# Performance work log

Hardware: AMD Instinct MI355X
Metric: run time of the kernel (lower is better)

Reference implementation:

```python
import jax, jax.numpy as jnp
import numpy as np

N, F, D = 32, 1024, 512
H = 2 * D  # dim * ratio
EPS = 1e-5


def batchnorm1d(x, gamma, beta):
    # x: (N, F, L); BatchNorm1d over channel dim F, stats over (N, L) (training mode, biased var)
    mean = jnp.mean(x, axis=(0, 2), keepdims=True)
    var = jnp.var(x, axis=(0, 2), keepdims=True)
    xn = (x - mean) * jax.lax.rsqrt(var + EPS)
    return xn * gamma[None, :, None] + beta[None, :, None]


def setup_inputs() -> dict:
    key = jax.random.key(0)
    ks = jax.random.split(key, 5)
    x = jax.random.normal(ks[0], (N, F, D), dtype=jnp.float32)
    W0 = jax.random.normal(ks[1], (H, D), dtype=jnp.float32) * 0.02  # Linear(D->H) weight (out,in)
    b0 = jnp.zeros((H,), jnp.float32)
    W1 = jax.random.normal(ks[2], (D, H), dtype=jnp.float32) * 0.02  # Linear(H->D)
    b1 = jnp.zeros((D,), jnp.float32)
    Wc = jax.random.normal(ks[3], (F, F), dtype=jnp.float32) * 0.02  # Conv1d k=1 weight (out_ch,in_ch)
    bc = jnp.zeros((F,), jnp.float32)
    ones = jnp.ones((F,), jnp.float32)
    zeros = jnp.zeros((F,), jnp.float32)
    return {
        "x": x,
        "W0": W0, "b0": b0, "g0": ones, "be0": zeros,
        "W1": W1, "b1": b1, "g1": ones, "be1": zeros,
        "gf": ones, "bf": zeros,
        "Wc": Wc, "bc": bc,
        "go": ones, "bo": zeros,
    }


def reference(x, W0, b0, g0, be0, W1, b1, g1, be1, gf, bf, Wc, bc, go, bo):
    # proj_mlp0: Linear(D->H) + BN1d(F)
    v = jnp.einsum('nfd,hd->nfh', x, W0) + b0  # (N, F, H)
    v = batchnorm1d(v, g0, be0)
    # correlation: bmm(v, v^T) -> softsign -> bmm(w, v)
    w = jnp.einsum('nfh,ngh->nfg', v, v)  # (N, F, F)
    w = w / (1.0 + jnp.abs(w))  # softsign
    v = jnp.einsum('nfg,ngh->nfh', w, v)  # (N, F, H)
    # proj_mlp1: Linear(H->D) + BN1d(F)
    v = jnp.einsum('nfh,dh->nfd', v, W1) + b1  # (N, F, D)
    v = batchnorm1d(v, g1, be1)
    # feed_norm(v + x)
    xr = batchnorm1d(v + x, gf, bf)
    # proj_conv: Conv1d(F->F, kernel=1) over channel dim
    v = jnp.einsum('oi,nid->nod', Wc, xr) + bc[None, :, None]
    return batchnorm1d(v + xr, go, bo)
```

## Files before the change

### kernel.cpp

```cpp
#include <hip/hip_runtime.h>
#include <stdint.h>

#define NB 32
#define FC 1024
#define DD 512
#define HH 1024
#define BN_EPS 1e-5f

typedef unsigned short u16;
typedef unsigned int u32;
typedef __attribute__((ext_vector_type(8))) short bf16x8;
typedef __attribute__((ext_vector_type(4))) float f32x4;
typedef __attribute__((ext_vector_type(8))) unsigned short ushort8v;

#define AS1 __attribute__((address_space(1)))
#define AS3 __attribute__((address_space(3)))

__device__ __forceinline__ float b2f(u16 u) {
    union { u32 i; float f; } v;
    v.i = ((u32)u) << 16;
    return v.f;
}
__device__ __forceinline__ u16 f2b(float f) {
    union { float f; u32 i; } v;
    v.f = f;
    const u32 b = v.i;
    return (u16)((b + 0x7FFFu + ((b >> 16) & 1u)) >> 16);
}

__device__ __forceinline__ void gld16(const u16* g, u16* l) {
    __builtin_amdgcn_global_load_lds((const AS1 u32*)g, (AS3 u32*)l, 16, 0, 0);
}

__device__ __forceinline__ void swizzle_tiles(int& mt, int& nt, int& zt) {
    const int gx = gridDim.x, gy = gridDim.y, gz = gridDim.z;
    const int mzTot = gy * gz;
    if ((mzTot & 7) != 0) { nt = blockIdx.x; mt = blockIdx.y; zt = blockIdx.z; return; }
    long lin = ((long)blockIdx.z * gy + blockIdx.y) * gx + blockIdx.x;
    const int slab = mzTot >> 3;
    const int xcd = (int)(lin & 7);
    const long idx = lin >> 3;
    nt = (int)(idx % gx);
    const int mz = (int)(idx / gx) + xcd * slab;
    mt = mz % gy;
    zt = mz / gy;
}

__global__ __launch_bounds__(256) void init_detect(
    float* __restrict__ sp, const u32* __restrict__ x, int* __restrict__ flag)
{
    sp[blockIdx.x * 256 + threadIdx.x] = 0.0f;
    if (blockIdx.x != 0) return;
    __shared__ int cnt[256];
    int c = 0;
    for (int i = threadIdx.x; i < 4096; i += 256) {
        const u32 lo = x[i] & 0xFFFFu;
        const u32 e = (lo >> 7) & 0xFFu;
        if (e >= 0x68u && e <= 0x85u) c++;
    }
    cnt[threadIdx.x] = c;
    __syncthreads();
    for (int s = 128; s > 0; s >>= 1) {
        if (threadIdx.x < (unsigned)s) cnt[threadIdx.x] += cnt[threadIdx.x + s];
        __syncthreads();
    }
    if (threadIdx.x == 0) flag[0] = (cnt[0] > 2048) ? 1 : 0;
}

__global__ __launch_bounds__(256) void fold_bn(
    const float* __restrict__ sp, const u16* __restrict__ gamma,
    const u16* __restrict__ beta, float* __restrict__ ssf, float invCnt)
{
    const int f = blockIdx.x * 256 + threadIdx.x;
    if (f < FC) {
        const float mean = sp[f] * invCnt;
        const float var  = sp[FC + f] * invCnt - mean * mean;
        const float rstd = rsqrtf(var + BN_EPS);
        const float sc   = b2f(gamma[f]) * rstd;
        ssf[f]      = sc;
        ssf[FC + f] = b2f(beta[f]) - mean * sc;
    }
}

__global__ __launch_bounds__(256) void fold2_bn(
    const float* __restrict__ sp1, const float* __restrict__ spx,
    const u16* __restrict__ g1, const u16* __restrict__ be1,
    const u16* __restrict__ gf, const u16* __restrict__ bf_,
    float* __restrict__ ssd, float cnt)
{
    const int f = blockIdx.x * 256 + threadIdx.x;
    if (f >= FC) return;
    const float inv  = 1.0f / cnt;
    const float S1v = sp1[f], S2v = sp1[FC + f], Sxv = sp1[2 * FC + f];
    const float mean1 = S1v * inv;
    const float var1  = S2v * inv - mean1 * mean1;
    const float sc1   = b2f(g1[f]) * rsqrtf(var1 + BN_EPS);
    const float sh1   = b2f(be1[f]) - mean1 * sc1;
    ssd[f]      = sc1;
    ssd[FC + f] = sh1;
    const float S1x = spx[f], S2x = spx[FC + f];
    const float sums = sc1 * S1v + cnt * sh1 + S1x;
    const float sss  = sc1 * sc1 * S2v + 2.f * sc1 * sh1 * S1v
                     + cnt * sh1 * sh1 + 2.f * sc1 * Sxv
                     + 2.f * sh1 * S1x + S2x;
    const float means = sums * inv;
    const float vars  = sss * inv - means * means;
    const float scf   = b2f(gf[f]) * rsqrtf(vars + BN_EPS);
    const float shf   = b2f(bf_[f]) - means * scf;
    ssd[2 * FC + f] = scf;
    ssd[3 * FC + f] = shf;
}

__global__ __launch_bounds__(256) void convert_x_stats(
    const void* __restrict__ src, u16* __restrict__ dst, long n4,
    const int* __restrict__ flag, float* __restrict__ spx)
{
    const bool isbf = (*flag != 0);
    long i4 = (long)blockIdx.x * blockDim.x + threadIdx.x;
    const long stride = (long)gridDim.x * blockDim.x;
    for (; i4 < n4; i4 += stride) {
        const long i = i4 << 2;
        ushort4 o;
        if (isbf) {
            o = *(const ushort4*)((const u16*)src + i);
        } else {
            const float4 v = *(const float4*)((const float*)src + i);
            o.x = f2b(v.x); o.y = f2b(v.y); o.z = f2b(v.z); o.w = f2b(v.w);
        }
        *(ushort4*)(dst + i) = o;
        const float a = b2f(o.x), b = b2f(o.y), c = b2f(o.z), d = b2f(o.w);
        float s1 = a + b + c + d;
        float s2 = a * a + b * b + c * c + d * d;
        #pragma unroll
        for (int m = 1; m < 64; m <<= 1) {
            s1 += __shfl_xor(s1, m);
            s2 += __shfl_xor(s2, m);
        }
        if ((threadIdx.x & 63) == 0) {
            const int ch = (int)((i >> 9) & (FC - 1));
            atomicAdd(&spx[ch], s1);
            atomicAdd(&spx[FC + ch], s2);
        }
    }
}

struct ConvArgs { const void* src[14]; long off[14]; long n4[14]; };
__global__ __launch_bounds__(256) void convert_params(
    ConvArgs a, u16* __restrict__ dst, const int* __restrict__ flag)
{
    const bool isbf = (*flag != 0);
    const long stride = (long)gridDim.x * blockDim.x;
    for (int s = 0; s < 14; ++s) {
        const long n4 = a.n4[s];
        u16* d = dst + a.off[s];
        const void* sp = a.src[s];
        for (long i4 = (long)blockIdx.x * blockDim.x + threadIdx.x; i4 < n4;
             i4 += stride) {
            const long i = i4 << 2;
            if (isbf) {
                *(ushort4*)(d + i) = *(const ushort4*)((const u16*)sp + i);
            } else {
                const float4 v = *(const float4*)((const float*)sp + i);
                ushort4 o;
                o.x = f2b(v.x); o.y = f2b(v.y); o.z = f2b(v.z); o.w = f2b(v.w);
                *(ushort4*)(d + i) = o;
            }
        }
    }
}

template<bool BIAS, bool SOFTSIGN, bool STATS, bool RESID, bool XSTAT>
__global__ __launch_bounds__(512, 4) void gemm128x256_nt(
    const u16* __restrict__ A, const u16* __restrict__ B,
    const u16* __restrict__ bias, const u16* __restrict__ resid,
    u16* __restrict__ C, float* __restrict__ sp,
    int M, int N, int K, int lda, int ldb, int ldc,
    long sA, long sB, long sC)
{
    extern __shared__ char smem[];

    int mt, nt, zt;
    swizzle_tiles(mt, nt, zt);
    const u16* Ab = A + (long)zt * sA + (long)(mt * 128) * lda;
    const u16* Bb = B + (long)zt * sB + (long)(nt * 256) * ldb;
    C += (long)zt * sC;
    const u16* RP = (RESID || XSTAT) ? (resid + (long)zt * sC) : nullptr;

    const int tid  = threadIdx.x;
    const int lane = tid & 63;
    const int wv   = tid >> 6;
    const int wrr  = (wv >> 2) * 64;
    const int wc   = (wv & 3) * 64;
    const int lm   = lane & 15;
    const int q    = lane >> 4;

    int aOff[4], bOff[4];
    #pragma unroll
    for (int i = 0; i < 4; ++i) {
        const int r = wrr + i * 16 + lm;
        aOff[i] = r * 64 + ((q ^ ((r >> 1) & 3)) << 4);
    }
    #pragma unroll
    for (int j = 0; j < 4; ++j) {
        const int r = wc + j * 16 + lm;
        bOff[j] = r * 64 + ((q ^ ((r >> 1) & 3)) << 4);
    }

    const int rw = lane >> 2, qs = lane & 3;
    const int rA  = wv * 16 + rw;
    const int rB0 = wv * 32 + rw;
    const int rB1 = wv * 32 + 16 + rw;
    const u16* pA  = Ab + (long)rA  * lda + ((qs ^ ((rA  >> 1) & 3)) << 3);
    const u16* pB0 = Bb + (long)rB0 * ldb + ((qs ^ ((rB0 >> 1) & 3)) << 3);
    const u16* pB1 = Bb + (long)rB1 * ldb + ((qs ^ ((rB1 >> 1) & 3)) << 3);
    const int ldsA  = wv * 1024;
    const int ldsB0 = wv * 2048;
    const int ldsB1 = wv * 2048 + 1024;

#define STAGE(bufOff, kofs) { \
    gld16(pA  + (kofs), (u16*)(smem + (bufOff) + ldsA)); \
    gld16(pB0 + (kofs), (u16*)(smem + (bufOff) + 8192 + ldsB0)); \
    gld16(pB1 + (kofs), (u16*)(smem + (bufOff) + 8192 + ldsB1)); }

    f32x4 acc[4][4] = {};

    const int NT = K >> 5;

    STAGE(0, 0);
    __syncthreads();

    for (int t = 0; t < NT; ++t) {
        const int bo = (t & 1) * 24576;
        const int bn = ((t + 1) & 1) * 24576;
        if (t + 1 < NT) STAGE(bn, (t + 1) * 32);

        bf16x8 a[4], b[4];
        const char* baseA = smem + bo;
        const char* baseB = smem + bo + 8192;
        #pragma unroll
        for (int i = 0; i < 4; ++i) a[i] = *(const bf16x8*)(baseA + aOff[i]);
        #pragma unroll
        for (int j = 0; j < 4; ++j) b[j] = *(const bf16x8*)(baseB + bOff[j]);

        #pragma unroll
        for (int i = 0; i < 4; ++i)
            #pragma unroll
            for (int j = 0; j < 4; ++j)
                acc[i][j] = __builtin_amdgcn_mfma_f32_16x16x32_bf16(
                    a[i], b[j], acc[i][j], 0, 0, 0);

        __syncthreads();
    }

#undef STAGE

    float* rep = (float*)smem + wv * (16 * 65);
    const int rr = lane >> 2;
    const int cg = lane & 3;
    const int m0 = mt * 128;
    const int n0 = nt * 256;
    #pragma unroll
    for (int i = 0; i < 4; ++i) {
        #pragma unroll
        for (int j = 0; j < 4; ++j) {
            const int col = 16 * j + lm;
            const float bj = BIAS ? b2f(bias[n0 + wc + col]) : 0.0f;
            #pragma unroll
            for (int r = 0; r < 4; ++r) {
                float v = acc[i][j][r] + bj;
                if (SOFTSIGN) v = v / (1.0f + fabsf(v));
                rep[(q * 4 + r) * 65 + col] = v;
            }
        }
        const int row = m0 + wrr + 16 * i + rr;
        const float* lr = rep + rr * 65 + cg * 16;
        float4 f0 = *(const float4*)(lr + 0);
        float4 f1 = *(const float4*)(lr + 4);
        float4 f2 = *(const float4*)(lr + 8);
        float4 f3 = *(const float4*)(lr + 12);
        ushort8v ra, rb;
        if (RESID || XSTAT) {
            const u16* rp = RP + (long)row * ldc + n0 + wc + cg * 16;
            ra = *(const ushort8v*)rp;
            rb = *(const ushort8v*)(rp + 8);
        }
        if (RESID) {
            f0.x += b2f(ra[0]); f0.y += b2f(ra[1]); f0.z += b2f(ra[2]); f0.w += b2f(ra[3]);
            f1.x += b2f(ra[4]); f1.y += b2f(ra[5]); f1.z += b2f(ra[6]); f1.w += b2f(ra[7]);
            f2.x += b2f(rb[0]); f2.y += b2f(rb[1]); f2.z += b2f(rb[2]); f2.w += b2f(rb[3]);
            f3.x += b2f(rb[4]); f3.y += b2f(rb[5]); f3.z += b2f(rb[6]); f3.w += b2f(rb[7]);
        }
        if (STATS) {
            float s1 = (f0.x + f0.y + f0.z + f0.w) + (f1.x + f1.y + f1.z + f1.w)
                     + (f2.x + f2.y + f2.z + f2.w) + (f3.x + f3.y + f3.z + f3.w);
            float s2 = f0.x*f0.x + f0.y*f0.y + f0.z*f0.z + f0.w*f0.w
                     + f1.x*f1.x + f1.y*f1.y + f1.z*f1.z + f1.w*f1.w
                     + f2.x*f2.x + f2.y*f2.y + f2.z*f2.z + f2.w*f2.w
                     + f3.x*f3.x + f3.y*f3.y + f3.z*f3.z + f3.w*f3.w;
            float sxv = 0.0f;
            if (XSTAT) {
                sxv = f0.x*b2f(ra[0]) + f0.y*b2f(ra[1]) + f0.z*b2f(ra[2]) + f0.w*b2f(ra[3])
                    + f1.x*b2f(ra[4]) + f1.y*b2f(ra[5]) + f1.z*b2f(ra[6]) + f1.w*b2f(ra[7])
                    + f2.x*b2f(rb[0]) + f2.y*b2f(rb[1]) + f2.z*b2f(rb[2]) + f2.w*b2f(rb[3])
                    + f3.x*b2f(rb[4]) + f3.y*b2f(rb[5]) + f3.z*b2f(rb[6]) + f3.w*b2f(rb[7]);
            }
            s1 += __shfl_xor(s1, 1); s1 += __shfl_xor(s1, 2);
            s2 += __shfl_xor(s2, 1); s2 += __shfl_xor(s2, 2);
            if (XSTAT) { sxv += __shfl_xor(sxv, 1); sxv += __shfl_xor(sxv, 2); }
            if (cg == 0) {
                const int ch = row & (FC - 1);
                atomicAdd(&sp[ch], s1);
                atomicAdd(&sp[FC + ch], s2);
                if (XSTAT) atomicAdd(&sp[2 * FC + ch], sxv);
            }
        }
        ushort8v o0, o1;
        o0[0] = f2b(f0.x); o0[1] = f2b(f0.y); o0[2] = f2b(f0.z); o0[3] = f2b(f0.w);
        o0[4] = f2b(f1.x); o0[5] = f2b(f1.y); o0[6] = f2b(f1.z); o0[7] = f2b(f1.w);
        o1[0] = f2b(f2.x); o1[1] = f2b(f2.y); o1[2] = f2b(f2.z); o1[3] = f2b(f2.w);
        o1[4] = f2b(f3.x); o1[5] = f2b(f3.y); o1[6] = f2b(f3.z); o1[7] = f2b(f3.w);
        u16* cp = C + (long)row * ldc + n0 + wc + cg * 16;
        *(ushort8v*)cp = o0;
        *(ushort8v*)(cp + 8) = o1;
    }
}

__global__ __launch_bounds__(256) void transpose_bn_bf16(
    const u16* __restrict__ src, u16* __restrict__ dstT,
    u16* __restrict__ dstI, const float* __restrict__ ssf,
    int R, int Cc, long sS, long sD)
{
    __shared__ u16 t[32][36];
    const int bz = blockIdx.z;
    src  += (long)bz * sS;
    dstI += (long)bz * sS;
    dstT += (long)bz * sD;
    const int c0 = blockIdx.x * 32;
    const int r0 = blockIdx.y * 32;
    const int lx = threadIdx.x & 7;
    const int ly = threadIdx.x >> 3;

    const int r = r0 + ly;
    const float sc = ssf[r];
    const float sh = ssf[FC + r];
    const ushort4 v = *(const ushort4*)(src + (long)r * Cc + c0 + lx * 4);
    ushort4 nv;
    nv.x = f2b(fmaf(b2f(v.x), sc, sh));
    nv.y = f2b(fmaf(b2f(v.y), sc, sh));
    nv.z = f2b(fmaf(b2f(v.z), sc, sh));
    nv.w = f2b(fmaf(b2f(v.w), sc, sh));
    *(ushort4*)(dstI + (long)r * Cc + c0 + lx * 4) = nv;
    *(ushort4*)&t[ly][lx * 4] = nv;

    __syncthreads();

    const int oc = c0 + ly;
    ushort4 o;
    o.x = t[lx * 4 + 0][ly];
    o.y = t[lx * 4 + 1][ly];
    o.z = t[lx * 4 + 2][ly];
    o.w = t[lx * 4 + 3][ly];
    *(ushort4*)(dstT + (long)oc * R + r0 + lx * 4) = o;
}

__global__ __launch_bounds__(256) void transpose_bn2_bf16(
    const u16* __restrict__ v3, const u16* __restrict__ x,
    u16* __restrict__ dstT, u16* __restrict__ dstI,
    const float* __restrict__ ssd, int R, int Cc, long sS, long sD)
{
    __shared__ u16 t[32][36];
    const int bz = blockIdx.z;
    v3   += (long)bz * sS;
    x    += (long)bz * sS;
    dstI += (long)bz * sS;
    dstT += (long)bz * sD;
    const int c0 = blockIdx.x * 32;
    const int r0 = blockIdx.y * 32;
    const int lx = threadIdx.x & 7;
    const int ly = threadIdx.x >> 3;

    const int r = r0 + ly;
    const float sc1 = ssd[r];
    const float sh1 = ssd[FC + r];
    const float scf = ssd[2 * FC + r];
    const float shf = ssd[3 * FC + r];
    const long base = (long)r * Cc + c0 + lx * 4;
    const ushort4 v  = *(const ushort4*)(v3 + base);
    const ushort4 xv = *(const ushort4*)(x + base);
    ushort4 nv;
    float s;
    s = fmaf(b2f(v.x), sc1, sh1) + b2f(xv.x); nv.x = f2b(fmaf(s, scf, shf));
    s = fmaf(b2f(v.y), sc1, sh1) + b2f(xv.y); nv.y = f2b(fmaf(s, scf, shf));
    s = fmaf(b2f(v.z), sc1, sh1) + b2f(xv.z); nv.z = f2b(fmaf(s, scf, shf));
    s = fmaf(b2f(v.w), sc1, sh1) + b2f(xv.w); nv.w = f2b(fmaf(s, scf, shf));
    *(ushort4*)(dstI + base) = nv;
    *(ushort4*)&t[ly][lx * 4] = nv;

    __syncthreads();

    const int oc = c0 + ly;
    ushort4 o;
    o.x = t[lx * 4 + 0][ly];
    o.y = t[lx * 4 + 1][ly];
    o.z = t[lx * 4 + 2][ly];
    o.w = t[lx * 4 + 3][ly];
    *(ushort4*)(dstT + (long)oc * R + r0 + lx * 4) = o;
}

__global__ __launch_bounds__(256) void bn_apply(
    const u16* __restrict__ src, const float* __restrict__ ss,
    void* __restrict__ dst, const int* __restrict__ outflag,
    long total4, int lcShift)
{
    const bool outf32 = (outflag != nullptr) && (*outflag == 0);
    long i4 = (long)blockIdx.x * blockDim.x + threadIdx.x;
    const long stride = (long)gridDim.x * blockDim.x;
    for (; i4 < total4; i4 += stride) {
        const long i = i4 << 2;
        const int c = (int)((i >> lcShift) & (FC - 1));
        const float sc = ss[c];
        const float sh = ss[FC + c];
        const ushort4 v = *(const ushort4*)(src + i);
        const float o0 = fmaf(b2f(v.x), sc, sh);
        const float o1 = fmaf(b2f(v.y), sc, sh);
        const float o2 = fmaf(b2f(v.z), sc, sh);
        const float o3 = fmaf(b2f(v.w), sc, sh);
        if (outf32) {
            float4 o; o.x = o0; o.y = o1; o.z = o2; o.w = o3;
            *(float4*)((float*)dst + i) = o;
        } else {
            ushort4 o;
            o.x = f2b(o0); o.y = f2b(o1); o.z = f2b(o2); o.w = f2b(o3);
            *(ushort4*)((u16*)dst + i) = o;
        }
    }
}

extern "C" void kernel_launch(void* const* d_in, const int* in_sizes, int n_in,
                              void* d_out, int out_size, void* d_ws, size_t ws_size,
                              hipStream_t stream)
{
    const size_t MiB = (size_t)1 << 20;
    const long sFH = (long)FC * HH;
    const long sFF = (long)FC * FC;
    const long sFD = (long)FC * DD;
    const long PE  = (long)NB * FC * DD;

    const size_t GLDS = 49152;
    static bool s_attr = false;
    if (!s_attr) {
        s_attr = true;
        hipFuncSetAttribute(reinterpret_cast<const void*>(&gemm128x256_nt<true, false, true, false, false>),
                            hipFuncAttributeMaxDynamicSharedMemorySize, (int)GLDS);
        hipFuncSetAttribute(reinterpret_cast<const void*>(&gemm128x256_nt<false, true, false, false, false>),
                            hipFuncAttributeMaxDynamicSharedMemorySize, (int)GLDS);
        hipFuncSetAttribute(reinterpret_cast<const void*>(&gemm128x256_nt<false, false, false, false, false>),
                            hipFuncAttributeMaxDynamicSharedMemorySize, (int)GLDS);
        hipFuncSetAttribute(reinterpret_cast<const void*>(&gemm128x256_nt<true, false, true, false, true>),
                            hipFuncAttributeMaxDynamicSharedMemorySize, (int)GLDS);
        hipFuncSetAttribute(reinterpret_cast<const void*>(&gemm128x256_nt<true, false, true, true, false>),
                            hipFuncAttributeMaxDynamicSharedMemorySize, (int)GLDS);
    }

    long off[16];
    long cur = 0;
    for (int i = 1; i < 15; ++i) { off[i] = cur; cur += ((long)in_sizes[i] + 7) & ~7L; }
    const size_t paramBytes = (size_t)cur * 2;

    int cb = 32;
    while (cb > 1 &&
           64 * MiB + (size_t)cb * 6 * MiB + paramBytes + 131072 > ws_size)
        cb >>= 1;

    u16* V   = (u16*)d_ws;
    u16* VT  = (u16*)((char*)d_ws + 64 * MiB);
    u16* WW  = VT + (long)cb * sFH;
    u16* V2  = WW + (long)cb * sFF;
    u16* WC  = V2 + (long)cb * sFH;
    char* tail = (char*)(WC + cur);
    tail = (char*)(((uintptr_t)tail + 255) & ~(uintptr_t)255);
    float* SP0  = (float*)tail;
    float* SP1  = SP0 + 2 * FC;
    float* SPX  = SP1 + 3 * FC;
    float* SP3  = SPX + 2 * FC;
    float* SSF  = SP3 + 2 * FC;
    float* SSD  = SSF + 2 * FC;
    int*   FLAG = (int*)(SSD + 4 * FC);
    u16* VX  = (u16*)d_out;
    u16* XB  = (u16*)d_out + PE;
    u16* V4  = V;
    u16* XRT = V + PE;

    const dim3 blk(256);
    const dim3 blk512(512);
    const dim3 egrid(4096);

    init_detect<<<dim3(36), blk, 0, stream>>>(SP0, (const u32*)d_in[0], FLAG);
    ConvArgs ca;
    for (int i = 1; i < 15; ++i) {
        ca.src[i - 1] = d_in[i];
        ca.off[i - 1] = off[i];
        ca.n4[i - 1]  = (long)in_sizes[i] / 4;
    }
    convert_params<<<dim3(256), blk, 0, stream>>>(ca, WC, FLAG);
    convert_x_stats<<<dim3(1024), blk, 0, stream>>>(d_in[0], XB, PE / 4, FLAG, SPX);

    const u16* W0c = WC + off[1];
    const u16* b0c = WC + off[2];
    const u16* g0c = WC + off[3];
    const u16* be0c = WC + off[4];
    const u16* W1c = WC + off[5];
    const u16* b1c = WC + off[6];
    const u16* g1c = WC + off[7];
    const u16* be1c = WC + off[8];
    const u16* gfc = WC + off[9];
    const u16* bfc = WC + off[10];
    const u16* Wcc = WC + off[11];
    const u16* bcc = WC + off[12];
    const u16* goc = WC + off[13];
    const u16* boc = WC + off[14];

    gemm128x256_nt<true, false, true, false, false><<<dim3(HH / 256, (NB * FC) / 128, 1), blk512, GLDS, stream>>>(
        XB, W0c, b0c, nullptr, V, SP0, NB * FC, HH, DD, DD, DD, HH, 0, 0, 0);
    fold_bn<<<dim3(4), blk, 0, stream>>>(SP0, g0c, be0c, SSF, 1.0f / (float)(NB * HH));

    for (int bz0 = 0; bz0 < NB; bz0 += cb) {
        const int c = (NB - bz0 < cb) ? (NB - bz0) : cb;
        transpose_bn_bf16<<<dim3(HH / 32, FC / 32, c), blk, 0, stream>>>(
            V + bz0 * sFH, VT, V + bz0 * sFH, SSF, FC, HH, sFH, sFH);
        gemm128x256_nt<false, true, false, false, false><<<dim3(FC / 256, FC / 128, c), blk512, GLDS, stream>>>(
            V + bz0 * sFH, V + bz0 * sFH, nullptr, nullptr, WW, nullptr,
            FC, FC, HH, HH, HH, FC, sFH, sFH, sFF);
        gemm128x256_nt<false, false, false, false, false><<<dim3(HH / 256, FC / 128, c), blk512, GLDS, stream>>>(
            WW, VT, nullptr, nullptr, V2, nullptr,
            FC, HH, FC, FC, FC, HH, sFF, sFH, sFH);
        gemm128x256_nt<true, false, true, false, true><<<dim3(DD / 256, (c * FC) / 128, 1), blk512, GLDS, stream>>>(
            V2, W1c, b1c, XB + bz0 * sFD, VX + bz0 * sFD, SP1,
            c * FC, DD, HH, HH, HH, DD, 0, 0, 0);
    }

    fold2_bn<<<dim3(4), blk, 0, stream>>>(SP1, SPX, g1c, be1c, gfc, bfc,
                                          SSD, (float)(NB * DD));

    transpose_bn2_bf16<<<dim3(DD / 32, FC / 32, NB), blk, 0, stream>>>(
        VX, XB, XRT, VX, SSD, FC, DD, sFD, sFD);

    gemm128x256_nt<true, false, true, true, false><<<dim3(DD / 256, FC / 128, NB), blk512, GLDS, stream>>>(
        Wcc, XRT, bcc, VX, V4, SP3, FC, DD, FC, FC, FC, DD, 0, sFD, sFD);
    fold_bn<<<dim3(4), blk, 0, stream>>>(SP3, goc, boc, SSF, 1.0f / (float)(NB * DD));

    bn_apply<<<egrid, blk, 0, stream>>>(V4, SSF, d_out, FLAG, PE / 4, 9);
}
```

Before: 591.5 us.

## Enlarge GEMM tiles to 256x256 with BK=64 and split staging

Replaces the 128x256 tile GEMM with a 256x256 tile that uses a 64-wide K step. A and B staging is split across two half-steps, with a new XOR LDS swizzle and s_setprio around the MFMA block. The aim is more MFMA work per byte loaded and fewer K-loop syncs. In exchange it uses 128KB of LDS and more accumulator registers, which lowers occupancy to about one block per CU, and halves the grid size.

Result: no change. 596.2 us (+0.8%).

```diff
diff --git a/kernel.cpp b/kernel.cpp
--- a/kernel.cpp
+++ b/kernel.cpp
@@ -170,7 +170,7 @@
 }
 
 template<bool BIAS, bool SOFTSIGN, bool STATS, bool RESID, bool XSTAT>
-__global__ __launch_bounds__(512, 4) void gemm128x256_nt(
+__global__ __launch_bounds__(512, 2) void gemm256_nt(
     const u16* __restrict__ A, const u16* __restrict__ B,
     const u16* __restrict__ bias, const u16* __restrict__ resid,
     u16* __restrict__ C, float* __restrict__ sp,
@@ -181,7 +181,7 @@
 
     int mt, nt, zt;
     swizzle_tiles(mt, nt, zt);
-    const u16* Ab = A + (long)zt * sA + (long)(mt * 128) * lda;
+    const u16* Ab = A + (long)zt * sA + (long)(mt * 256) * lda;
     const u16* Bb = B + (long)zt * sB + (long)(nt * 256) * ldb;
     C += (long)zt * sC;
     const u16* RP = (RESID || XSTAT) ? (resid + (long)zt * sC) : nullptr;
@@ -189,78 +189,94 @@
     const int tid  = threadIdx.x;
     const int lane = tid & 63;
     const int wv   = tid >> 6;
-    const int wrr  = (wv >> 2) * 64;
+    const int wr   = (wv >> 2) * 128;
     const int wc   = (wv & 3) * 64;
     const int lm   = lane & 15;
     const int q    = lane >> 4;
 
-    int aOff[4], bOff[4];
+    int aOff[8][2], bOff[4][2];
     #pragma unroll
-    for (int i = 0; i < 4; ++i) {
-        const int r = wrr + i * 16 + lm;
-        aOff[i] = r * 64 + ((q ^ ((r >> 1) & 3)) << 4);
+    for (int i = 0; i < 8; ++i) {
+        const int r = wr + i * 16 + lm;
+        #pragma unroll
+        for (int kh = 0; kh < 2; ++kh)
+            aOff[i][kh] = r * 128 + (((kh * 4 + q) ^ (r & 7)) << 4);
     }
     #pragma unroll
     for (int j = 0; j < 4; ++j) {
         const int r = wc + j * 16 + lm;
-        bOff[j] = r * 64 + ((q ^ ((r >> 1) & 3)) << 4);
-    }
-
-    const int rw = lane >> 2, qs = lane & 3;
-    const int rA  = wv * 16 + rw;
-    const int rB0 = wv * 32 + rw;
-    const int rB1 = wv * 32 + 16 + rw;
-    const u16* pA  = Ab + (long)rA  * lda + ((qs ^ ((rA  >> 1) & 3)) << 3);
-    const u16* pB0 = Bb + (long)rB0 * ldb + ((qs ^ ((rB0 >> 1) & 3)) << 3);
-    const u16* pB1 = Bb + (long)rB1 * ldb + ((qs ^ ((rB1 >> 1) & 3)) << 3);
-    const int ldsA  = wv * 1024;
-    const int ldsB0 = wv * 2048;
-    const int ldsB1 = wv * 2048 + 1024;
-
-#define STAGE(bufOff, kofs) { \
-    gld16(pA  + (kofs), (u16*)(smem + (bufOff) + ldsA)); \
-    gld16(pB0 + (kofs), (u16*)(smem + (bufOff) + 8192 + ldsB0)); \
-    gld16(pB1 + (kofs), (u16*)(smem + (bufOff) + 8192 + ldsB1)); }
-
-    f32x4 acc[4][4] = {};
-
-    const int NT = K >> 5;
-
-    STAGE(0, 0);
+        #pragma unroll
+        for (int kh = 0; kh < 2; ++kh)
+            bOff[j][kh] = r * 128 + (((kh * 4 + q) ^ (r & 7)) << 4);
+    }
+
+    const int rL  = lane >> 3;
+    const int gsw = ((lane & 7) ^ rL) << 3;
+    const u16* pAs = Ab + (long)(wv * 32 + rL) * lda + gsw;
+    const u16* pBs = Bb + (long)(wv * 32 + rL) * ldb + gsw;
+    const int ldsRow0 = wv * 32 * 128;
+
+#define STAGE_A(bufOff, kofs) { \
+    gld16(pAs + 0 * 8 * lda + (kofs), (u16*)(smem + (bufOff) + ldsRow0 + 0 * 1024)); \
+    gld16(pAs + 1 * 8 * lda + (kofs), (u16*)(smem + (bufOff) + ldsRow0 + 1 * 1024)); \
+    gld16(pAs + 2 * 8 * lda + (kofs), (u16*)(smem + (bufOff) + ldsRow0 + 2 * 1024)); \
+    gld16(pAs + 3 * 8 * lda + (kofs), (u16*)(smem + (bufOff) + ldsRow0 + 3 * 1024)); }
+#define STAGE_B(bufOff, kofs) { \
+    gld16(pBs + 0 * 8 * ldb + (kofs), (u16*)(smem + (bufOff) + 32768 + ldsRow0 + 0 * 1024)); \
+    gld16(pBs + 1 * 8 * ldb + (kofs), (u16*)(smem + (bufOff) + 32768 + ldsRow0 + 1 * 1024)); \
+    gld16(pBs + 2 * 8 * ldb + (kofs), (u16*)(smem + (bufOff) + 32768 + ldsRow0 + 2 * 1024)); \
+    gld16(pBs + 3 * 8 * ldb + (kofs), (u16*)(smem + (bufOff) + 32768 + ldsRow0 + 3 * 1024)); }
+
+    f32x4 acc[8][4] = {};
+
+    const int NT = K >> 6;
+
+    STAGE_A(0, 0); STAGE_B(0, 0);
     __syncthreads();
 
     for (int t = 0; t < NT; ++t) {
-        const int bo = (t & 1) * 24576;
-        const int bn = ((t + 1) & 1) * 24576;
-        if (t + 1 < NT) STAGE(bn, (t + 1) * 32);
-
-        bf16x8 a[4], b[4];
-        const char* baseA = smem + bo;
-        const char* baseB = smem + bo + 8192;
+        const int bo = (t & 1) * 65536;
+        const int bn = ((t + 1) & 1) * 65536;
+        const int kn = (t + 1) * 64;
+        const bool pf = (t + 1 < NT);
+
         #pragma unroll
-        for (int i = 0; i < 4; ++i) a[i] = *(const bf16x8*)(baseA + aOff[i]);
-        #pragma unroll
-        for (int j = 0; j < 4; ++j) b[j] = *(const bf16x8*)(baseB + bOff[j]);
-
-        #pragma unroll
-        for (int i = 0; i < 4; ++i)
+        for (int kh = 0; kh < 2; ++kh) {
+            if (pf) {
+                if (kh == 0) STAGE_A(bn, kn)
+                else         STAGE_B(bn, kn)
+            }
+            bf16x8 a[8], b[4];
+            const char* baseA = smem + bo;
+            const char* baseB = smem + bo + 32768;
             #pragma unroll
-            for (int j = 0; j < 4; ++j)
-                acc[i][j] = __builtin_amdgcn_mfma_f32_16x16x32_bf16(
-                    a[i], b[j], acc[i][j], 0, 0, 0);
+            for (int i = 0; i < 8; ++i) a[i] = *(const bf16x8*)(baseA + aOff[i][kh]);
+            #pragma unroll
+            for (int j = 0; j < 4; ++j) b[j] = *(const bf16x8*)(baseB + bOff[j][kh]);
+
+            __builtin_amdgcn_s_setprio(1);
+            #pragma unroll
+            for (int i = 0; i < 8; ++i)
+                #pragma unroll
+                for (int j = 0; j < 4; ++j)
+                    acc[i][j] = __builtin_amdgcn_mfma_f32_16x16x32_bf16(
+                        a[i], b[j], acc[i][j], 0, 0, 0);
+            __builtin_amdgcn_s_setprio(0);
+        }
 
         __syncthreads();
     }
 
-#undef STAGE
+#undef STAGE_A
+#undef STAGE_B
 
     float* rep = (float*)smem + wv * (16 * 65);
     const int rr = lane >> 2;
     const int cg = lane & 3;
-    const int m0 = mt * 128;
+    const int m0 = mt * 256;
     const int n0 = nt * 256;
     #pragma unroll
-    for (int i = 0; i < 4; ++i) {
+    for (int i = 0; i < 8; ++i) {
         #pragma unroll
         for (int j = 0; j < 4; ++j) {
             const int col = 16 * j + lm;
@@ -272,7 +288,7 @@
                 rep[(q * 4 + r) * 65 + col] = v;
             }
         }
-        const int row = m0 + wrr + 16 * i + rr;
+        const int row = m0 + wr + 16 * i + rr;
         const float* lr = rep + rr * 65 + cg * 16;
         float4 f0 = *(const float4*)(lr + 0);
         float4 f1 = *(const float4*)(lr + 4);
@@ -446,19 +462,19 @@
     const long sFD = (long)FC * DD;
     const long PE  = (long)NB * FC * DD;
 
-    const size_t GLDS = 49152;
+    const size_t GLDS = 131072;
     static bool s_attr = false;
     if (!s_attr) {
         s_attr = true;
-        hipFuncSetAttribute(reinterpret_cast<const void*>(&gemm128x256_nt<true, false, true, false, false>),
+        hipFuncSetAttribute(reinterpret_cast<const void*>(&gemm256_nt<true, false, true, false, false>),
                             hipFuncAttributeMaxDynamicSharedMemorySize, (int)GLDS);
-        hipFuncSetAttribute(reinterpret_cast<const void*>(&gemm128x256_nt<false, true, false, false, false>),
+        hipFuncSetAttribute(reinterpret_cast<const void*>(&gemm256_nt<false, true, false, false, false>),
                             hipFuncAttributeMaxDynamicSharedMemorySize, (int)GLDS);
-        hipFuncSetAttribute(reinterpret_cast<const void*>(&gemm128x256_nt<false, false, false, false, false>),
+        hipFuncSetAttribute(reinterpret_cast<const void*>(&gemm256_nt<false, false, false, false, false>),
                             hipFuncAttributeMaxDynamicSharedMemorySize, (int)GLDS);
-        hipFuncSetAttribute(reinterpret_cast<const void*>(&gemm128x256_nt<true, false, true, false, true>),
+        hipFuncSetAttribute(reinterpret_cast<const void*>(&gemm256_nt<true, false, true, false, true>),
                             hipFuncAttributeMaxDynamicSharedMemorySize, (int)GLDS);
-        hipFuncSetAttribute(reinterpret_cast<const void*>(&gemm128x256_nt<true, false, true, true, false>),
+        hipFuncSetAttribute(reinterpret_cast<const void*>(&gemm256_nt<true, false, true, true, false>),
                             hipFuncAttributeMaxDynamicSharedMemorySize, (int)GLDS);
     }
 
@@ -520,7 +536,7 @@
     const u16* goc = WC + off[13];
     const u16* boc = WC + off[14];
 
-    gemm128x256_nt<true, false, true, false, false><<<dim3(HH / 256, (NB * FC) / 128, 1), blk512, GLDS, stream>>>(
+    gemm256_nt<true, false, true, false, false><<<dim3(HH / 256, (NB * FC) / 256, 1), blk512, GLDS, stream>>>(
         XB, W0c, b0c, nullptr, V, SP0, NB * FC, HH, DD, DD, DD, HH, 0, 0, 0);
     fold_bn<<<dim3(4), blk, 0, stream>>>(SP0, g0c, be0c, SSF, 1.0f / (float)(NB * HH));
 
@@ -528,13 +544,13 @@
         const int c = (NB - bz0 < cb) ? (NB - bz0) : cb;
         transpose_bn_bf16<<<dim3(HH / 32, FC / 32, c), blk, 0, stream>>>(
             V + bz0 * sFH, VT, V + bz0 * sFH, SSF, FC, HH, sFH, sFH);
-        gemm128x256_nt<false, true, false, false, false><<<dim3(FC / 256, FC / 128, c), blk512, GLDS, stream>>>(
+        gemm256_nt<false, true, false, false, false><<<dim3(FC / 256, FC / 256, c), blk512, GLDS, stream>>>(
             V + bz0 * sFH, V + bz0 * sFH, nullptr, nullptr, WW, nullptr,
             FC, FC, HH, HH, HH, FC, sFH, sFH, sFF);
-        gemm128x256_nt<false, false, false, false, false><<<dim3(HH / 256, FC / 128, c), blk512, GLDS, stream>>>(
+        gemm256_nt<false, false, false, false, false><<<dim3(HH / 256, FC / 256, c), blk512, GLDS, stream>>>(
             WW, VT, nullptr, nullptr, V2, nullptr,
             FC, HH, FC, FC, FC, HH, sFF, sFH, sFH);
-        gemm128x256_nt<true, false, true, false, true><<<dim3(DD / 256, (c * FC) / 128, 1), blk512, GLDS, stream>>>(
+        gemm256_nt<true, false, true, false, true><<<dim3(DD / 256, (c * FC) / 256, 1), blk512, GLDS, stream>>>(
             V2, W1c, b1c, XB + bz0 * sFD, VX + bz0 * sFD, SP1,
             c * FC, DD, HH, HH, HH, DD, 0, 0, 0);
     }
@@ -545,7 +561,7 @@
     transpose_bn2_bf16<<<dim3(DD / 32, FC / 32, NB), blk, 0, stream>>>(
         VX, XB, XRT, VX, SSD, FC, DD, sFD, sFD);
 
-    gemm128x256_nt<true, false, true, true, false><<<dim3(DD / 256, FC / 128, NB), blk512, GLDS, stream>>>(
+    gemm256_nt<true, false, true, true, false><<<dim3(DD / 256, FC / 256, NB), blk512, GLDS, stream>>>(
         Wcc, XRT, bcc, VX, V4, SP3, FC, DD, FC, FC, FC, DD, 0, sFD, sFD);
     fold_bn<<<dim3(4), blk, 0, stream>>>(SP3, goc, boc, SSF, 1.0f / (float)(NB * DD));
 
```
